# Performance work log

Hardware: AMD Instinct MI355X
Metric: run time of the kernel (lower is better)

Reference implementation:

```python
import jax, jax.numpy as jnp
import numpy as np

B, C, T = 128, 8, 128   # batch, channels, time steps
K, S = 20, 128          # known classes, barycenter length


def setup_inputs() -> dict:
    key = jax.random.key(0)
    k1, k2, k3, k4, k5 = jax.random.split(key, 5)
    x = jax.random.normal(k1, (B, C, T), dtype=jnp.float32)
    preds = jax.random.randint(k2, (B,), 0, K).astype(jnp.int32)
    barycenters = jax.random.normal(k3, (K, S, C), dtype=jnp.float32)
    # thresholds centered near realistic scales so both detector branches fire
    top_dist = 7.0 + 0.5 * jax.random.normal(k4, (K,), dtype=jnp.float32)
    bottom_cc = 25.0 + 5.0 * jax.random.normal(k5, (K, C), dtype=jnp.float32)
    return {"x": x, "preds": preds, "barycenters": barycenters,
            "top_dist": top_dist, "bottom_cc": bottom_cc}


def _dtw_dist(cost):
    """Classic DTW DP over a [T, S] sq-euclidean cost matrix; returns accumulated cost."""
    inf = jnp.asarray(jnp.inf, cost.dtype)
    row0 = jnp.cumsum(cost[0])  # first row: only left moves

    def row_step(prev, crow):
        prev_shift = jnp.concatenate([jnp.full((1,), inf, cost.dtype), prev[:-1]])
        def col_step(left, inp):
            c, p, ps = inp
            v = c + jnp.minimum(jnp.minimum(p, ps), left)
            return v, v
        _, row = jax.lax.scan(col_step, inf, (crow, prev, prev_shift))
        return row, None

    last, _ = jax.lax.scan(row_step, row0, cost[1:])
    return last[-1]


def reference(x, preds, barycenters, top_dist, bottom_cc):
    xt = jnp.transpose(x, (0, 2, 1))                    # [B, T, C]
    x2 = jnp.sum(xt * xt, axis=-1)                      # [B, T]
    b2 = jnp.sum(barycenters * barycenters, axis=-1)    # [K, S]
    dots = jnp.einsum('btc,ksc->bkts', xt, barycenters)  # [B, K, T, S]
    cost = jnp.maximum(x2[:, None, :, None] + b2[None, :, None, :] - 2.0 * dots, 0.0)

    Bn, Kn, Tn, Sn = cost.shape
    dists = jax.vmap(_dtw_dist)(cost.reshape(Bn * Kn, Tn, Sn)).reshape(Bn, Kn)
    log_dists = jnp.log(dists)
    dtw_unknown = jnp.all(log_dists > top_dist[None, :], axis=1)   # [B]

    # per-channel full cross-correlation max vs each barycenter
    corr_max = lambda a, v: jnp.max(jnp.correlate(a, v, mode='full'))
    per_ch = jax.vmap(corr_max, in_axes=(1, 1))          # over channels -> [C]
    per_cls = jax.vmap(per_ch, in_axes=(None, 0))        # over classes  -> [K, C]
    per_b = jax.vmap(per_cls, in_axes=(0, None))         # over batch    -> [B, K, C]
    ccs = per_b(xt, barycenters)
    # class 'fails' if any channel cc is not above its bottom threshold
    cc_unknown = jnp.all(jnp.any(ccs <= bottom_cc[None, :, :], axis=2), axis=1)  # [B]

    unknown = cc_unknown | dtw_unknown
    return jnp.where(unknown, Kn, preds)
```

## Files before the change

### kernel.cpp

```cpp
#include <hip/hip_runtime.h>
#include <hip/hip_bf16.h>
#include <math.h>

#define B_ 128
#define C_ 8
#define T_ 128
#define K_ 20
#define S_ 128

#define XROW 388
#define BTROW 132
#define SWZ(j) ((j) ^ ((((j) >> 5) & 7) << 2))
#define XP_GUARD 16
#define BT_BASE (4 * XROW + XP_GUARD)
#define DTW_TILE 1152
#define SMEMF 4608

__device__ __forceinline__ float dpp_shr1(float v) {
    int r = __builtin_amdgcn_update_dpp(0, __float_as_int(v), 0x111, 0xf, 0xf, true);
    return __int_as_float(r);
}

__global__ __launch_bounds__(256) void fused_kernel(const float* __restrict__ x,
                                                    const float* __restrict__ bary,
                                                    const float* __restrict__ top_dist,
                                                    const float* __restrict__ bottom_cc,
                                                    int* __restrict__ dtw_gt,
                                                    int* __restrict__ cc_fail2) {
    __shared__ __align__(16) float smem[SMEMF];
    const float INF = __builtin_inff();
    int u = blockIdx.x;
    int tid = threadIdx.x;
    int w = tid >> 6;
    int lane = tid & 63;

    if (u % 9 == 0) {
        int pg = (u / 9) * 4 + w;
        int b  = pg / 5;
        int kg = pg - b * 5;
        int g  = lane >> 4;
        int gl = lane & 15;
        int ks = kg * 4 + g;
        float* tile = smem + w * DTW_TILE;

        const float* xb_ = x + (size_t)b * (C_ * T_);
        #pragma unroll
        for (int r = 0; r < 4; ++r) {
            int f = r * 64 + lane;
            int c = f >> 5;
            int t0 = (f & 31) * 4;
            float4 v = *(const float4*)(xb_ + c * T_ + t0);
            float* dst = tile + (c >> 2) * 512 + (c & 3);
            dst[(t0 + 0) * 4] = v.x;
            dst[(t0 + 1) * 4] = v.y;
            dst[(t0 + 2) * 4] = v.z;
            dst[(t0 + 3) * 4] = v.w;
        }
        __syncthreads();
        #pragma unroll
        for (int r = 0; r < 2; ++r) {
            int t = r * 64 + lane;
            float4 xa = *(const float4*)(tile + t * 4);
            float4 xh = *(const float4*)(tile + 512 + t * 4);
            float s = xa.x * xa.x;
            s = fmaf(xa.y, xa.y, s); s = fmaf(xa.z, xa.z, s); s = fmaf(xa.w, xa.w, s);
            s = fmaf(xh.x, xh.x, s); s = fmaf(xh.y, xh.y, s); s = fmaf(xh.z, xh.z, s);
            s = fmaf(xh.w, xh.w, s);
            tile[1024 + t] = s;
        }
        __syncthreads();

        float bv[8][8], B2s[8];
        {
            const float4* bp = (const float4*)(bary + (size_t)ks * (S_ * C_) + 64 * gl);
            #pragma unroll
            for (int r = 0; r < 8; ++r) {
                float4 q0 = bp[2 * r], q1 = bp[2 * r + 1];
                bv[r][0] = q0.x; bv[r][1] = q0.y; bv[r][2] = q0.z; bv[r][3] = q0.w;
                bv[r][4] = q1.x; bv[r][5] = q1.y; bv[r][6] = q1.z; bv[r][7] = q1.w;
                float s = 0.f;
                #pragma unroll
                for (int ch = 0; ch < 8; ++ch) s = fmaf(bv[r][ch], bv[r][ch], s);
                B2s[r] = s;
                #pragma unroll
                for (int ch = 0; ch < 8; ++ch) bv[r][ch] *= -2.f;
            }
        }

        float cr[8];
        #pragma unroll
        for (int i = 0; i < 8; ++i) cr[i] = INF;
        bool is0 = (gl == 0);
        float lcp = is0 ? 0.f : INF;

        const float* tX2 = tile + 1024;
        for (int d = 0; d < T_ + 15; ++d) {
            float lc = dpp_shr1(cr[7]);
            lc = is0 ? INF : lc;
            int t = d - gl;
            int tc = t < 0 ? 0 : (t > T_ - 1 ? T_ - 1 : t);
            float bse = tX2[tc];
            float4 xa = *(const float4*)(tile + tc * 4);
            float4 xh = *(const float4*)(tile + 512 + tc * 4);
            float xv[8];
            xv[0] = xa.x; xv[1] = xa.y; xv[2] = xa.z; xv[3] = xa.w;
            xv[4] = xh.x; xv[5] = xh.y; xv[6] = xh.z; xv[7] = xh.w;
            float a[8];
            #pragma unroll
            for (int r = 0; r < 8; ++r) {
                float ar = bse + B2s[r];
                #pragma unroll
                for (int ch = 0; ch < 8; ++ch) ar = fmaf(bv[r][ch], xv[ch], ar);
                a[r] = fmaxf(ar, 0.f);
            }
            float diag = lcp, left = lc;
            #pragma unroll
            for (int r = 0; r < 8; ++r) {
                float n = a[r] + fminf(fminf(cr[r], diag), left);
                diag = cr[r];
                cr[r] = n;
                left = n;
            }
            lcp = lc;
        }

        if (gl == 15)
            dtw_gt[b * K_ + ks] = (logf(cr[7]) > top_dist[ks]) ? 1 : 0;
    } else {
        int cb = u - u / 9 - 1;
        int bh = cb / 5;
        int g5 = cb - bh * 5;
        int b  = bh >> 1;
        int h  = bh & 1;
        int kk = g5 * 4 + w;
        int cbase = h * 4;

        float* xp = smem;
        float* bt = smem + BT_BASE + w * (4 * BTROW);

        const float* xsrc = x + ((size_t)b * C_ + cbase) * T_;
        #pragma unroll
        for (int c = 0; c < 4; ++c) {
            for (int j = tid; j < XROW; j += 256) {
                int t = j - (S_ - 1);
                float v = (t >= 0 && t < T_) ? xsrc[c * T_ + t] : 0.f;
                xp[c * XROW + SWZ(j)] = v;
            }
        }
        #pragma unroll
        for (int r = 0; r < 2; ++r) {
            int s = r * 64 + lane;
            float4 q = *(const float4*)(bary + ((size_t)kk * S_ + s) * C_ + cbase);
            bt[0 * BTROW + s] = q.x;
            bt[1 * BTROW + s] = q.y;
            bt[2 * BTROW + s] = q.z;
            bt[3 * BTROW + s] = q.w;
        }
        __syncthreads();

        int cl = lane >> 4;
        int gl = lane & 15;
        int lag0 = gl << 4;
        const float* xr = xp + cl * XROW;
        const float* br = bt + cl * BTROW;

        float wdw[20];
        #pragma unroll
        for (int i = 0; i < 5; ++i) {
            float4 v = *(const float4*)&xr[SWZ(lag0 + i * 4)];
            wdw[i * 4 + 0] = v.x; wdw[i * 4 + 1] = v.y;
            wdw[i * 4 + 2] = v.z; wdw[i * 4 + 3] = v.w;
        }
        float acc[16];
        #pragma unroll
        for (int j = 0; j < 16; ++j) acc[j] = 0.f;

        #pragma unroll 8
        for (int s4 = 0; s4 < S_; s4 += 4) {
            float4 bq = *(const float4*)&br[s4];
            float bvals[4] = {bq.x, bq.y, bq.z, bq.w};
            #pragma unroll
            for (int uu = 0; uu < 4; ++uu) {
                #pragma unroll
                for (int j = 0; j < 16; ++j)
                    acc[j] = fmaf(wdw[uu + j], bvals[uu], acc[j]);
            }
            #pragma unroll
            for (int i = 0; i < 16; ++i) wdw[i] = wdw[i + 4];
            float4 v = *(const float4*)&xr[SWZ(lag0 + s4 + 20)];
            wdw[16] = v.x; wdw[17] = v.y; wdw[18] = v.z; wdw[19] = v.w;
        }

        if (gl == 15) acc[15] = -INF;
        float m = acc[0];
        #pragma unroll
        for (int j = 1; j < 16; ++j) m = fmaxf(m, acc[j]);
        #pragma unroll
        for (int off = 8; off >= 1; off >>= 1)
            m = fmaxf(m, __shfl_xor(m, off));

        bool fail = false;
        if (gl == 0) fail = (m <= bottom_cc[kk * C_ + cbase + cl]);
        unsigned long long bal = __ballot(fail);
        if (lane == 0) cc_fail2[(b * K_ + kk) * 2 + h] = (bal != 0ULL) ? 1 : 0;
    }
}

__global__ void final_kernel(const int* __restrict__ preds,
                             const int* __restrict__ dtw_gt,
                             const int* __restrict__ cc_fail2,
                             int* __restrict__ out) {
    int b = threadIdx.x;
    if (b < B_) {
        int dtw_all = 1, cc_all = 1;
        #pragma unroll
        for (int k = 0; k < K_; ++k) {
            dtw_all &= dtw_gt[b * K_ + k];
            cc_all &= (cc_fail2[(b * K_ + k) * 2] | cc_fail2[(b * K_ + k) * 2 + 1]);
        }
        out[b] = (dtw_all | cc_all) ? K_ : preds[b];
    }
}

extern "C" void kernel_launch(void* const* d_in, const int* in_sizes, int n_in,
                              void* d_out, int out_size, void* d_ws, size_t ws_size,
                              hipStream_t stream) {
    const float* x         = (const float*)d_in[0];
    const int*   preds     = (const int*)d_in[1];
    const float* bary      = (const float*)d_in[2];
    const float* top_dist  = (const float*)d_in[3];
    const float* bottom_cc = (const float*)d_in[4];
    int* out = (int*)d_out;

    int* dtw_gt   = (int*)d_ws;
    int* cc_fail2 = dtw_gt + B_ * K_;

    fused_kernel<<<1440, 256, 0, stream>>>(x, bary, top_dist, bottom_cc, dtw_gt, cc_fail2);
    final_kernel<<<1, 128, 0, stream>>>(preds, dtw_gt, cc_fail2, out);
}
```

Baseline: 67.01 us.

## Spread DTW wavefront across full wave with 2 columns per lane

Restructures the DTW anti-diagonal DP so each 64-lane wave handles one (batch, class) pair, with each lane owning 2 barycenter columns instead of 16-lane groups owning 8 columns each. The x time-step values are streamed across lanes via wave-wide DPP shift, injected at lane 0, rather than each lane reading LDS. This shortens the serial per-step chain from 8 dependent mins to 2, at the cost of more diagonal steps (T+63 vs T+15). The grid grows and the DTW/cross-correlation block split changes from 1:8 to 1:2, so four times as many blocks run the DTW path.

```diff
diff --git a/kernel.cpp b/kernel.cpp
--- a/kernel.cpp
+++ b/kernel.cpp
@@ -13,11 +13,11 @@
 #define SWZ(j) ((j) ^ ((((j) >> 5) & 7) << 2))
 #define XP_GUARD 16
 #define BT_BASE (4 * XROW + XP_GUARD)
-#define DTW_TILE 1152
-#define SMEMF 4608
-
-__device__ __forceinline__ float dpp_shr1(float v) {
-    int r = __builtin_amdgcn_update_dpp(0, __float_as_int(v), 0x111, 0xf, 0xf, true);
+#define SMEMF 3680
+
+__device__ __forceinline__ float dpp_wshr1(float inj, float v) {
+    int r = __builtin_amdgcn_update_dpp(__float_as_int(inj), __float_as_int(v),
+                                        0x138, 0xf, 0xf, false);
     return __int_as_float(r);
 }
 
@@ -34,22 +34,17 @@
     int w = tid >> 6;
     int lane = tid & 63;
 
-    if (u % 9 == 0) {
-        int pg = (u / 9) * 4 + w;
+    if (u % 3 == 0) {
+        int pg = u / 3;
         int b  = pg / 5;
         int kg = pg - b * 5;
-        int g  = lane >> 4;
-        int gl = lane & 15;
-        int ks = kg * 4 + g;
-        float* tile = smem + w * DTW_TILE;
-
-        const float* xb_ = x + (size_t)b * (C_ * T_);
-        #pragma unroll
-        for (int r = 0; r < 4; ++r) {
-            int f = r * 64 + lane;
-            int c = f >> 5;
-            int t0 = (f & 31) * 4;
-            float4 v = *(const float4*)(xb_ + c * T_ + t0);
+        int kk = kg * 4 + w;
+        float* tile = smem;
+
+        {
+            int c  = tid >> 5;
+            int t0 = (tid & 31) * 4;
+            float4 v = *(const float4*)(x + ((size_t)b * C_ + c) * T_ + t0);
             float* dst = tile + (c >> 2) * 512 + (c & 3);
             dst[(t0 + 0) * 4] = v.x;
             dst[(t0 + 1) * 4] = v.y;
@@ -57,9 +52,8 @@
             dst[(t0 + 3) * 4] = v.w;
         }
         __syncthreads();
-        #pragma unroll
-        for (int r = 0; r < 2; ++r) {
-            int t = r * 64 + lane;
+        if (tid < T_) {
+            int t = tid;
             float4 xa = *(const float4*)(tile + t * 4);
             float4 xh = *(const float4*)(tile + 512 + t * 4);
             float s = xa.x * xa.x;
@@ -70,64 +64,72 @@
         }
         __syncthreads();
 
-        float bv[8][8], B2s[8];
+        float bv0[8], bv1[8], B20, B21;
         {
-            const float4* bp = (const float4*)(bary + (size_t)ks * (S_ * C_) + 64 * gl);
-            #pragma unroll
-            for (int r = 0; r < 8; ++r) {
-                float4 q0 = bp[2 * r], q1 = bp[2 * r + 1];
-                bv[r][0] = q0.x; bv[r][1] = q0.y; bv[r][2] = q0.z; bv[r][3] = q0.w;
-                bv[r][4] = q1.x; bv[r][5] = q1.y; bv[r][6] = q1.z; bv[r][7] = q1.w;
-                float s = 0.f;
-                #pragma unroll
-                for (int ch = 0; ch < 8; ++ch) s = fmaf(bv[r][ch], bv[r][ch], s);
-                B2s[r] = s;
-                #pragma unroll
-                for (int ch = 0; ch < 8; ++ch) bv[r][ch] *= -2.f;
-            }
-        }
-
-        float cr[8];
-        #pragma unroll
-        for (int i = 0; i < 8; ++i) cr[i] = INF;
-        bool is0 = (gl == 0);
-        float lcp = is0 ? 0.f : INF;
-
-        const float* tX2 = tile + 1024;
-        for (int d = 0; d < T_ + 15; ++d) {
-            float lc = dpp_shr1(cr[7]);
-            lc = is0 ? INF : lc;
-            int t = d - gl;
-            int tc = t < 0 ? 0 : (t > T_ - 1 ? T_ - 1 : t);
-            float bse = tX2[tc];
-            float4 xa = *(const float4*)(tile + tc * 4);
-            float4 xh = *(const float4*)(tile + 512 + tc * 4);
-            float xv[8];
-            xv[0] = xa.x; xv[1] = xa.y; xv[2] = xa.z; xv[3] = xa.w;
-            xv[4] = xh.x; xv[5] = xh.y; xv[6] = xh.z; xv[7] = xh.w;
-            float a[8];
-            #pragma unroll
-            for (int r = 0; r < 8; ++r) {
-                float ar = bse + B2s[r];
-                #pragma unroll
-                for (int ch = 0; ch < 8; ++ch) ar = fmaf(bv[r][ch], xv[ch], ar);
-                a[r] = fmaxf(ar, 0.f);
-            }
-            float diag = lcp, left = lc;
-            #pragma unroll
-            for (int r = 0; r < 8; ++r) {
-                float n = a[r] + fminf(fminf(cr[r], diag), left);
-                diag = cr[r];
-                cr[r] = n;
-                left = n;
-            }
+            const float4* bp = (const float4*)(bary + ((size_t)kk * S_ + 2 * lane) * C_);
+            float4 q0 = bp[0], q1 = bp[1], q2 = bp[2], q3 = bp[3];
+            bv0[0]=q0.x; bv0[1]=q0.y; bv0[2]=q0.z; bv0[3]=q0.w;
+            bv0[4]=q1.x; bv0[5]=q1.y; bv0[6]=q1.z; bv0[7]=q1.w;
+            bv1[0]=q2.x; bv1[1]=q2.y; bv1[2]=q2.z; bv1[3]=q2.w;
+            bv1[4]=q3.x; bv1[5]=q3.y; bv1[6]=q3.z; bv1[7]=q3.w;
+            float s0 = 0.f, s1 = 0.f;
+            #pragma unroll
+            for (int ch = 0; ch < 8; ++ch) {
+                s0 = fmaf(bv0[ch], bv0[ch], s0);
+                s1 = fmaf(bv1[ch], bv1[ch], s1);
+            }
+            B20 = s0; B21 = s1;
+            #pragma unroll
+            for (int ch = 0; ch < 8; ++ch) { bv0[ch] *= -2.f; bv1[ch] *= -2.f; }
+        }
+
+        float xv[8], xz = 0.f, inj[8], iz = 0.f;
+        #pragma unroll
+        for (int i = 0; i < 8; ++i) { xv[i] = 0.f; inj[i] = 0.f; }
+        if (lane == 0) {
+            float4 xa = *(const float4*)(tile);
+            float4 xh = *(const float4*)(tile + 512);
+            inj[0]=xa.x; inj[1]=xa.y; inj[2]=xa.z; inj[3]=xa.w;
+            inj[4]=xh.x; inj[5]=xh.y; inj[6]=xh.z; inj[7]=xh.w;
+            iz = tile[1024];
+        }
+
+        float c0 = INF, c1 = INF;
+        float lcp = (lane == 0) ? 0.f : INF;
+
+        for (int d = 0; d < T_ + 63; ++d) {
+            #pragma unroll
+            for (int i = 0; i < 8; ++i) xv[i] = dpp_wshr1(inj[i], xv[i]);
+            xz = dpp_wshr1(iz, xz);
+            float lc = dpp_wshr1(INF, c1);
+
+            if (lane == 0) {
+                int tn = (d + 1 < T_) ? d + 1 : T_ - 1;
+                float4 xa = *(const float4*)(tile + tn * 4);
+                float4 xh = *(const float4*)(tile + 512 + tn * 4);
+                inj[0]=xa.x; inj[1]=xa.y; inj[2]=xa.z; inj[3]=xa.w;
+                inj[4]=xh.x; inj[5]=xh.y; inj[6]=xh.z; inj[7]=xh.w;
+                iz = tile[1024 + tn];
+            }
+
+            float a0 = xz + B20, a1 = xz + B21;
+            #pragma unroll
+            for (int ch = 0; ch < 8; ++ch) {
+                a0 = fmaf(bv0[ch], xv[ch], a0);
+                a1 = fmaf(bv1[ch], xv[ch], a1);
+            }
+            a0 = fmaxf(a0, 0.f);
+            a1 = fmaxf(a1, 0.f);
+            float n0 = a0 + fminf(fminf(c0, lcp), lc);
+            float n1 = a1 + fminf(fminf(c1, c0), n0);
+            c0 = n0; c1 = n1;
             lcp = lc;
         }
 
-        if (gl == 15)
-            dtw_gt[b * K_ + ks] = (logf(cr[7]) > top_dist[ks]) ? 1 : 0;
+        if (lane == 63)
+            dtw_gt[b * K_ + kk] = (logf(c1) > top_dist[kk]) ? 1 : 0;
     } else {
-        int cb = u - u / 9 - 1;
+        int cb = u - u / 3 - 1;
         int bh = cb / 5;
         int g5 = cb - bh * 5;
         int b  = bh >> 1;
@@ -235,6 +237,6 @@
     int* dtw_gt   = (int*)d_ws;
     int* cc_fail2 = dtw_gt + B_ * K_;
 
-    fused_kernel<<<1440, 256, 0, stream>>>(x, bary, top_dist, bottom_cc, dtw_gt, cc_fail2);
+    fused_kernel<<<1920, 256, 0, stream>>>(x, bary, top_dist, bottom_cc, dtw_gt, cc_fail2);
     final_kernel<<<1, 128, 0, stream>>>(preds, dtw_gt, cc_fail2, out);
 }
```

New measurement: 82.04 us. 22.4% more time.
